# Kernel optimization log

Measured on AMD Instinct MI355X. Metric: run time of the kernel, lower is better.

The kernel has to match this reference:

```python
import jax, jax.numpy as jnp
import numpy as np

B, S, D, H, DH, F = 2, 2048, 1024, 16, 64, 4096
K = 2048  # number of selected tokens (capacity_gamma=0.5 of B*S)
EPS = 1e-6
ROPE_THETA = 10000.0


def setup_inputs() -> dict:
    key = jax.random.key(0)
    ks = jax.random.split(key, 12)
    w = lambda k, shp: jax.random.normal(k, shp, dtype=jnp.float32) * 0.02
    # K unique flat indices into the B*S token grid (every other token -> unique, sorted)
    sel_flat = jnp.arange(K, dtype=jnp.int64) * 2
    return {
        "hidden_states": jax.random.normal(ks[0], (B, S, D), dtype=jnp.float32),
        "gating_signal": jax.random.uniform(ks[1], (B, S), dtype=jnp.float32),
        "sel_flat": sel_flat,
        "position_ids": jnp.tile(jnp.arange(S, dtype=jnp.int64), (B, 1)),
        "ln1_w": jnp.ones((D,), jnp.float32),
        "ln2_w": jnp.ones((D,), jnp.float32),
        "wq": w(ks[2], (D, H * DH)), "bq": jnp.zeros((H * DH,), jnp.float32),
        "wk": w(ks[3], (D, H * DH)), "bk": jnp.zeros((H * DH,), jnp.float32),
        "wv": w(ks[4], (D, H * DH)), "bv": jnp.zeros((H * DH,), jnp.float32),
        "wo": w(ks[5], (H * DH, D)),
        "w_gate": w(ks[6], (D, F)),
        "w_up": w(ks[7], (D, F)),
        "w_down": w(ks[8], (F, D)),
    }


def _rmsnorm(x, w):
    var = jnp.mean(jnp.square(x), axis=-1, keepdims=True)
    return x * jax.lax.rsqrt(var + EPS) * w


def _rope(x, pos):
    # x: [K, H, DH], pos: [K]
    half = DH // 2
    inv_freq = 1.0 / (ROPE_THETA ** (jnp.arange(half, dtype=jnp.float32) / half))
    ang = pos.astype(jnp.float32)[:, None] * inv_freq  # [K, half]
    cos = jnp.cos(ang)[:, None, :]
    sin = jnp.sin(ang)[:, None, :]
    x1, x2 = x[..., :half], x[..., half:]
    return jnp.concatenate([x1 * cos - x2 * sin, x2 * cos + x1 * sin], axis=-1)


def reference(hidden_states, gating_signal, sel_flat, position_ids,
              ln1_w, ln2_w, wq, bq, wk, bk, wv, bv, wo, w_gate, w_up, w_down):
    b_idx = sel_flat // S
    t_idx = sel_flat % S

    # --- gather selected tokens ---
    x = hidden_states[b_idx, t_idx]          # [K, D]
    g = gating_signal[b_idx, t_idx]          # [K]
    pos = position_ids[b_idx, t_idx]         # [K]

    # --- Qwen2 block on the selected tokens (single sequence of length K) ---
    h = _rmsnorm(x, ln1_w)
    q = _rope((h @ wq + bq).reshape(K, H, DH), pos)
    k = _rope((h @ wk + bk).reshape(K, H, DH), pos)
    v = (h @ wv + bv).reshape(K, H, DH)

    scores = jnp.einsum("qhd,khd->hqk", q, k) / np.sqrt(DH)  # [H, K, K]
    causal = jnp.tril(jnp.ones((K, K), dtype=bool))
    scores = jnp.where(causal, scores, jnp.finfo(scores.dtype).min)
    probs = jax.nn.softmax(scores, axis=-1)
    attn = jnp.einsum("hqk,khd->qhd", probs, v).reshape(K, H * DH) @ wo

    x1 = x + attn
    h2 = _rmsnorm(x1, ln2_w)
    mlp = (jax.nn.silu(h2 @ w_gate) * (h2 @ w_up)) @ w_down
    y = x1 + mlp                              # processed tokens [K, D]

    # --- gated residual scatter-back ---
    updated = x + (y - x) * g[:, None]
    return hidden_states.at[b_idx, t_idx].set(updated)
```

## Files before the change

### kernel.cpp

```cpp
#include <hip/hip_runtime.h>
#include <hip/hip_bf16.h>
#include <stdint.h>

#define K_TOK 2048
#define D_DIM 1024
#define H_N   16
#define DH_N  64
#define F_DIM 4096
#define S_SEQ 2048

typedef __attribute__((ext_vector_type(4))) float f32x4;
typedef __attribute__((ext_vector_type(8))) short bf16x8;

__device__ __forceinline__ float bf2f(ushort u) {
  union { unsigned u; float f; } c; c.u = ((unsigned)u) << 16; return c.f;
}
__device__ __forceinline__ ushort f2bf(float f) {
  union { float f; unsigned u; } c; c.f = f;
  unsigned x = c.u + 0x7fffu + ((c.u >> 16) & 1u);
  return (ushort)(x >> 16);
}

#define GLOAD_LDS16(GP, LP)                                                   \
  __builtin_amdgcn_global_load_lds(                                           \
      (const __attribute__((address_space(1))) unsigned int*)(GP),            \
      (__attribute__((address_space(3))) unsigned int*)(LP), 16, 0, 0)

__global__ void copy_out_k(const float4* __restrict__ src, float4* __restrict__ dst, int n4) {
  int idx = blockIdx.x * blockDim.x + threadIdx.x;
  int stride = gridDim.x * blockDim.x;
  for (; idx < n4; idx += stride) dst[idx] = src[idx];
}

__global__ void prep_bias(const float* __restrict__ bq, const float* __restrict__ bk,
                          const float* __restrict__ bv, float* __restrict__ dst) {
  int i = blockIdx.x * 256 + threadIdx.x;
  if (i < 3072) dst[i] = (i < 1024) ? bq[i] : (i < 2048 ? bk[i - 1024] : bv[i - 2048]);
}

__global__ __launch_bounds__(256) void transpose_conv(const float* __restrict__ src,
                                                      ushort* __restrict__ dst,
                                                      int R, int C, int mul, int add, int ldd) {
  __shared__ float tile[32][33];
  int nbx = C >> 5;
  int bx = blockIdx.x % nbx, by = blockIdx.x / nbx;
  int c0 = bx << 5, r0 = by << 5;
  int tx = threadIdx.x & 31, ty = threadIdx.x >> 5;
#pragma unroll
  for (int i = 0; i < 32; i += 8)
    tile[ty + i][tx] = src[(size_t)(r0 + ty + i) * C + c0 + tx];
  __syncthreads();
#pragma unroll
  for (int i = 0; i < 32; i += 8) {
    int c = ty + i;
    dst[(size_t)((c0 + c) * mul + add) * ldd + r0 + tx] = f2bf(tile[tx][c]);
  }
}

__global__ __launch_bounds__(256) void gather_ln1(
    const float* __restrict__ hs, const float* __restrict__ gating,
    const int* __restrict__ sel32, const int* __restrict__ pos32,
    const float* __restrict__ w,
    float* __restrict__ xbuf, ushort* __restrict__ hbuf,
    float* __restrict__ gbuf, int* __restrict__ rowb, int* __restrict__ rowt,
    int* __restrict__ rowpos) {
  int i = blockIdx.x, tid = threadIdx.x;
  __shared__ float red[4];
  bool is64 = (sel32[1] == 0 && sel32[3] == 0 && sel32[5] == 0);
  int sel = is64 ? sel32[2 * i] : sel32[i];
  int b = sel >> 11;
  int t = sel & 2047;
  const float4* src = (const float4*)(hs + ((size_t)b * S_SEQ + t) * D_DIM);
  float4 v = src[tid];
  float ss = v.x * v.x + v.y * v.y + v.z * v.z + v.w * v.w;
  for (int off = 32; off; off >>= 1) ss += __shfl_xor(ss, off);
  if ((tid & 63) == 0) red[tid >> 6] = ss;
  __syncthreads();
  float tot = red[0] + red[1] + red[2] + red[3];
  float rms = rsqrtf(tot * (1.f / 1024.f) + 1e-6f);
  ((float4*)(xbuf + (size_t)i * D_DIM))[tid] = v;
  float4 lw = ((const float4*)w)[tid];
  ushort4 hv;
  hv.x = f2bf(v.x * rms * lw.x); hv.y = f2bf(v.y * rms * lw.y);
  hv.z = f2bf(v.z * rms * lw.z); hv.w = f2bf(v.w * rms * lw.w);
  *(ushort4*)&hbuf[(size_t)i * D_DIM + tid * 4] = hv;
  if (tid == 0) {
    rowb[i] = b; rowt[i] = t;
    bool is64p = (pos32[1] == 0 && pos32[3] == 0 && pos32[5] == 0);
    int pidx = b * S_SEQ + t;
    rowpos[i] = is64p ? pos32[2 * pidx] : pos32[pidx];
    gbuf[i] = gating[pidx];
  }
}

__global__ __launch_bounds__(256) void rmsnorm_ep1(const float* __restrict__ xbuf,
                                                   const float* __restrict__ pb,
                                                   const float* __restrict__ w,
                                                   float* __restrict__ x1out,
                                                   ushort* __restrict__ h2out) {
  int i = blockIdx.x, tid = threadIdx.x;
  __shared__ float red[4];
  size_t e = (size_t)i * D_DIM;
  float4 v = ((const float4*)(xbuf + e))[tid];
  float4 p0 = ((const float4*)(pb + e))[tid];
  float4 p1 = ((const float4*)(pb + 2097152 + e))[tid];
  v.x += p0.x + p1.x; v.y += p0.y + p1.y; v.z += p0.z + p1.z; v.w += p0.w + p1.w;
  ((float4*)(x1out + e))[tid] = v;
  float ss = v.x * v.x + v.y * v.y + v.z * v.z + v.w * v.w;
  for (int off = 32; off; off >>= 1) ss += __shfl_xor(ss, off);
  if ((tid & 63) == 0) red[tid >> 6] = ss;
  __syncthreads();
  float tot = red[0] + red[1] + red[2] + red[3];
  float rms = rsqrtf(tot * (1.f / 1024.f) + 1e-6f);
  float4 lw = ((const float4*)w)[tid];
  ushort4 hv;
  hv.x = f2bf(v.x * rms * lw.x); hv.y = f2bf(v.y * rms * lw.y);
  hv.z = f2bf(v.z * rms * lw.z); hv.w = f2bf(v.w * rms * lw.w);
  *(ushort4*)&h2out[e + tid * 4] = hv;
}

__global__ __launch_bounds__(256) void ep3_k(const float* __restrict__ pb,
                                             const float* __restrict__ x1b,
                                             const float* __restrict__ xbuf,
                                             const float* __restrict__ gbuf,
                                             const int* __restrict__ rowb,
                                             const int* __restrict__ rowt,
                                             float* __restrict__ out) {
  int idx = blockIdx.x * 256 + threadIdx.x;
  int row = idx >> 8, c4 = idx & 255;
  size_t e = (size_t)row * D_DIM + c4 * 4;
  float4 s0 = *(const float4*)(pb + e);
  float4 s1 = *(const float4*)(pb + 2097152 + e);
  float4 s2 = *(const float4*)(pb + 2 * 2097152 + e);
  float4 s3 = *(const float4*)(pb + 3 * 2097152 + e);
  float4 x = *(const float4*)(xbuf + e);
  float4 x1 = *(const float4*)(x1b + e);
  float g = gbuf[row];
  float4 r;
  r.x = x.x + (x1.x + s0.x + s1.x + s2.x + s3.x - x.x) * g;
  r.y = x.y + (x1.y + s0.y + s1.y + s2.y + s3.y - x.y) * g;
  r.z = x.z + (x1.z + s0.z + s1.z + s2.z + s3.z - x.z) * g;
  r.w = x.w + (x1.w + s0.w + s1.w + s2.w + s3.w - x.w) * g;
  *(float4*)(out + ((size_t)rowb[row] * S_SEQ + rowt[row]) * D_DIM + c4 * 4) = r;
}

template <int MODE>
__global__ __launch_bounds__(256) void gemm_bt(
    const ushort* __restrict__ A, const ushort* __restrict__ BT,
    int M, int N, int ldk, int kdeff, int per,
    const float* __restrict__ bias,
    ushort* __restrict__ outb, float* __restrict__ outf) {
  __shared__ ushort lA[128 * 64];
  __shared__ ushort lB[128 * 64];
  int tid = threadIdx.x;
  int lane = tid & 63, wid = tid >> 6;
  int kidx = blockIdx.x / per;
  int bid = blockIdx.x % per;
  int nbn = N >> 7;
  int tm = bid / nbn, tn = bid % nbn;
  int wr = wid >> 1, wc = wid & 1;
  f32x4 acc[4][4];
#pragma unroll
  for (int m = 0; m < 4; ++m)
#pragma unroll
    for (int n = 0; n < 4; ++n) acc[m][n] = (f32x4){0.f, 0.f, 0.f, 0.f};

  const ushort* Ab = A + (size_t)(tm * 128) * ldk + (size_t)kidx * kdeff;
  const ushort* Bb = BT + (size_t)(tn * 128) * ldk + (size_t)kidx * kdeff;
  int lr = lane & 15, lg = lane >> 4;
  int prow = lane >> 3;
  int pch = lane & 7;

  for (int k0 = 0; k0 < kdeff; k0 += 64) {
    __syncthreads();
#pragma unroll
    for (int p = 0; p < 4; ++p) {
      int row = p * 32 + wid * 8 + prow;
      int g = pch ^ (row & 7);
      GLOAD_LDS16(Ab + (size_t)row * ldk + k0 + g * 8, &lA[(p * 32 + wid * 8) * 64]);
      GLOAD_LDS16(Bb + (size_t)row * ldk + k0 + g * 8, &lB[(p * 32 + wid * 8) * 64]);
    }
    __syncthreads();
#pragma unroll
    for (int ks = 0; ks < 2; ++ks) {
      bf16x8 af[4], bfv[4];
#pragma unroll
      for (int m = 0; m < 4; ++m) {
        int row = wr * 64 + m * 16 + lr;
        af[m] = *(const bf16x8*)((const char*)lA + row * 128 +
                                 ((ks * 64 + lg * 16) ^ ((row & 7) << 4)));
      }
#pragma unroll
      for (int n = 0; n < 4; ++n) {
        int row = wc * 64 + n * 16 + lr;
        bfv[n] = *(const bf16x8*)((const char*)lB + row * 128 +
                                  ((ks * 64 + lg * 16) ^ ((row & 7) << 4)));
      }
#pragma unroll
      for (int m = 0; m < 4; ++m)
#pragma unroll
        for (int n = 0; n < 4; ++n)
          acc[m][n] = __builtin_amdgcn_mfma_f32_16x16x32_bf16(af[m], bfv[n], acc[m][n], 0, 0, 0);
    }
  }

#pragma unroll
  for (int m = 0; m < 4; ++m) {
#pragma unroll
    for (int n = 0; n < 4; ++n) {
#pragma unroll
      for (int r = 0; r < 4; ++r) {
        int gr = tm * 128 + wr * 64 + m * 16 + lg * 4 + r;
        int gc = tn * 128 + wc * 64 + n * 16 + lr;
        float val = acc[m][n][r];
        if (MODE == 0) {
          outb[(size_t)gr * N + gc] = f2bf(val + bias[gc]);
        } else if (MODE == 2) {
          float other = __shfl_xor(val, 1);
          if (!(lane & 1)) {
            float g = val, u = other;
            float a = g / (1.f + __expf(-g)) * u;
            outb[(size_t)gr * (size_t)(N >> 1) + (gc >> 1)] = f2bf(a);
          }
        } else {
          outf[((size_t)kidx * M + gr) * N + gc] = val;
        }
      }
    }
  }
}

__global__ __launch_bounds__(256) void rope_kernel(const ushort* __restrict__ qkv,
                                                   const int* __restrict__ rowpos,
                                                   ushort* __restrict__ qr,
                                                   ushort* __restrict__ kr) {
  int idx = blockIdx.x * 256 + threadIdx.x;
  int i = idx >> 9;
  int rem = idx & 511;
  int h = rem >> 5, d = rem & 31;
  float pos = (float)rowpos[i];
  float inv = __expf(-(float)d * (9.210340371976184f / 32.0f));
  float ang = pos * inv;
  float sn, cs;
  __sincosf(ang, &sn, &cs);
  size_t base = (size_t)i * 3072;
  float q1 = bf2f(qkv[base + h * 64 + d]);
  float q2 = bf2f(qkv[base + h * 64 + 32 + d]);
  float k1 = bf2f(qkv[base + 1024 + h * 64 + d]);
  float k2 = bf2f(qkv[base + 1024 + h * 64 + 32 + d]);
  size_t ob = ((size_t)h * K_TOK + i) * DH_N;
  qr[ob + d] = f2bf((q1 * cs - q2 * sn) * 0.125f);
  qr[ob + 32 + d] = f2bf((q2 * cs + q1 * sn) * 0.125f);
  kr[ob + d] = f2bf(k1 * cs - k2 * sn);
  kr[ob + 32 + d] = f2bf(k2 * cs + k1 * sn);
}

__global__ __launch_bounds__(256) void vtrans_k(const ushort* __restrict__ qkv,
                                                ushort* __restrict__ vt) {
  __shared__ ushort tile[32][33];
  int bx = blockIdx.x & 63, by = blockIdx.x >> 6;
  int i0 = bx << 5, c0 = by << 5;
  int tx = threadIdx.x & 31, ty = threadIdx.x >> 5;
#pragma unroll
  for (int j = 0; j < 32; j += 8)
    tile[ty + j][tx] = qkv[(size_t)(i0 + ty + j) * 3072 + 2048 + c0 + tx];
  __syncthreads();
#pragma unroll
  for (int j = 0; j < 32; j += 8)
    vt[(size_t)(c0 + ty + j) * K_TOK + i0 + tx] = tile[tx][ty + j];
}

__global__ __launch_bounds__(256) void attn_mfma(const ushort* __restrict__ qr,
                                                 const ushort* __restrict__ kr,
                                                 const ushort* __restrict__ vt,
                                                 ushort* __restrict__ ows,
                                                 float* __restrict__ mlws) {
  __shared__ ushort ktile[2][64 * 64];
  __shared__ ushort vtile[2][64 * 64];
  __shared__ ushort pbuf[4][16 * 64];
  int tid = threadIdx.x, lane = tid & 63, wid = tid >> 6;
  int bid = blockIdx.x;
  int h = bid / 144;
  int rem = 143 - (bid % 144);
  int g = 0;
  while (rem >= 2 * (g + 1) * (g + 2)) ++g;
  int rem2 = rem - 2 * g * (g + 1);
  int qt = (g << 2) + rem2 / (g + 1);
  int ci = rem2 % (g + 1);
  int slot = h * 144 + rem;
  int q0 = qt << 6;
  int t0 = ci << 2;
  int t1 = min(t0 + 3, qt);

  const ushort* Kh = kr + (size_t)h * K_TOK * DH_N;
  const ushort* Vh = vt + (size_t)h * DH_N * K_TOK;
  int lr = lane & 15, lg = lane >> 4;
  int qbase = q0 + wid * 16;

  bf16x8 qf[2];
  const ushort* Qp = qr + ((size_t)h * K_TOK + qbase + lr) * DH_N + lg * 8;
  qf[0] = *(const bf16x8*)(Qp);
  qf[1] = *(const bf16x8*)(Qp + 32);

  f32x4 oa[4];
  float mreg[4], lreg[4];
#pragma unroll
  for (int ct = 0; ct < 4; ++ct) oa[ct] = (f32x4){0.f, 0.f, 0.f, 0.f};
#pragma unroll
  for (int r = 0; r < 4; ++r) { mreg[r] = -1e30f; lreg[r] = 0.f; }

  char* pws = (char*)&pbuf[wid][0];
  int srow8 = lane >> 3, schunk = lane & 7;

  auto stage = [&](int bi, int kb) {
#pragma unroll
    for (int j = 0; j < 2; ++j) {
      int rbase = wid * 16 + j * 8;
      int row = rbase + srow8;
      int gch = schunk ^ (row & 7);
      GLOAD_LDS16(Kh + (size_t)(kb + row) * DH_N + gch * 8, &ktile[bi][rbase * 64]);
      GLOAD_LDS16(Vh + (size_t)row * K_TOK + kb + gch * 8, &vtile[bi][rbase * 64]);
    }
  };

  stage(0, t0 << 6);
  int cur = 0;
  for (int t = t0; t <= t1; ++t) {
    int kb = t << 6;
    __syncthreads();
    if (t < t1) stage(cur ^ 1, (t + 1) << 6);

    const char* kt = (const char*)&ktile[cur][0];
    const char* vtl = (const char*)&vtile[cur][0];

    f32x4 sa[4];
#pragma unroll
    for (int ct = 0; ct < 4; ++ct) sa[ct] = (f32x4){0.f, 0.f, 0.f, 0.f};
#pragma unroll
    for (int s = 0; s < 2; ++s) {
#pragma unroll
      for (int ct = 0; ct < 4; ++ct) {
        int row = ct * 16 + lr;
        bf16x8 kf = *(const bf16x8*)(kt + row * 128 + ((s * 64 + lg * 16) ^ ((row & 7) << 4)));
        sa[ct] = __builtin_amdgcn_mfma_f32_16x16x32_bf16(qf[s], kf, sa[ct], 0, 0, 0);
      }
    }

#pragma unroll
    for (int r = 0; r < 4; ++r) {
      int q = qbase + lg * 4 + r;
      int prow = lg * 4 + r;
      float sv[4];
      float mx = mreg[r];
#pragma unroll
      for (int ct = 0; ct < 4; ++ct) {
        int key = kb + ct * 16 + lr;
        float x = sa[ct][r];
        sv[ct] = (key <= q) ? x : -1e30f;
        mx = fmaxf(mx, sv[ct]);
      }
      mx = fmaxf(mx, __shfl_xor(mx, 1));
      mx = fmaxf(mx, __shfl_xor(mx, 2));
      mx = fmaxf(mx, __shfl_xor(mx, 4));
      mx = fmaxf(mx, __shfl_xor(mx, 8));
      float resc = __expf(mreg[r] - mx);
      float ps = 0.f;
#pragma unroll
      for (int ct = 0; ct < 4; ++ct) {
        float p = __expf(sv[ct] - mx);
        ps += p;
        *(ushort*)(pws + prow * 128 + ((ct * 32 + lr * 2) ^ ((prow & 7) << 4))) = f2bf(p);
      }
      ps += __shfl_xor(ps, 1);
      ps += __shfl_xor(ps, 2);
      ps += __shfl_xor(ps, 4);
      ps += __shfl_xor(ps, 8);
      lreg[r] = lreg[r] * resc + ps;
      mreg[r] = mx;
#pragma unroll
      for (int ct = 0; ct < 4; ++ct) oa[ct][r] *= resc;
    }

    bf16x8 pf[2];
#pragma unroll
    for (int s = 0; s < 2; ++s)
      pf[s] = *(const bf16x8*)(pws + lr * 128 + ((s * 64 + lg * 16) ^ ((lr & 7) << 4)));
#pragma unroll
    for (int s = 0; s < 2; ++s) {
#pragma unroll
      for (int ct = 0; ct < 4; ++ct) {
        int row = ct * 16 + lr;
        bf16x8 vf = *(const bf16x8*)(vtl + row * 128 + ((s * 64 + lg * 16) ^ ((row & 7) << 4)));
        oa[ct] = __builtin_amdgcn_mfma_f32_16x16x32_bf16(pf[s], vf, oa[ct], 0, 0, 0);
      }
    }
    cur ^= 1;
  }

#pragma unroll
  for (int ct = 0; ct < 4; ++ct) {
#pragma unroll
    for (int r = 0; r < 4; ++r) {
      int prow = wid * 16 + lg * 4 + r;
      ows[(size_t)slot * 4096 + prow * 64 + ct * 16 + lr] = f2bf(oa[ct][r]);
    }
  }
  if (lr == 0) {
#pragma unroll
    for (int r = 0; r < 4; ++r) {
      int prow = wid * 16 + lg * 4 + r;
      mlws[(size_t)slot * 128 + prow] = mreg[r];
      mlws[(size_t)slot * 128 + 64 + prow] = lreg[r];
    }
  }
}

__global__ __launch_bounds__(256) void attn_combine(const ushort* __restrict__ ows,
                                                    const float* __restrict__ mlws,
                                                    ushort* __restrict__ aout) {
  int bid = blockIdx.x;
  int h = bid & 15, qt = bid >> 4;
  int g = qt >> 2;
  int nc = g + 1;
  int base = h * 144 + 2 * g * (g + 1) + (qt & 3) * nc;
  int tid = threadIdx.x;
  int row = tid >> 2, c0 = (tid & 3) * 16;
  float M = -1e30f;
  for (int i = 0; i < nc; ++i)
    M = fmaxf(M, mlws[(size_t)(base + i) * 128 + row]);
  float L = 0.f;
  float acc[16];
#pragma unroll
  for (int j = 0; j < 16; ++j) acc[j] = 0.f;
  for (int i = 0; i < nc; ++i) {
    size_t sl = (size_t)(base + i);
    float w = __expf(mlws[sl * 128 + row] - M);
    L += mlws[sl * 128 + 64 + row] * w;
    const bf16x8* op = (const bf16x8*)(ows + sl * 4096 + row * 64 + c0);
    bf16x8 v0 = op[0], v1 = op[1];
#pragma unroll
    for (int j = 0; j < 8; ++j) acc[j] += bf2f(((ushort)v0[j])) * w;
#pragma unroll
    for (int j = 0; j < 8; ++j) acc[8 + j] += bf2f(((ushort)v1[j])) * w;
  }
  float inv = 1.f / L;
  int q = qt * 64 + row;
  ushort* dst = aout + (size_t)q * D_DIM + h * DH_N + c0;
#pragma unroll
  for (int j = 0; j < 16; ++j) dst[j] = f2bf(acc[j] * inv);
}

extern "C" void kernel_launch(void* const* d_in, const int* in_sizes, int n_in,
                              void* d_out, int out_size, void* d_ws, size_t ws_size,
                              hipStream_t stream) {
  const float* hs = (const float*)d_in[0];
  const float* gating = (const float*)d_in[1];
  const int* sel32 = (const int*)d_in[2];
  const int* pos32 = (const int*)d_in[3];
  const float* ln1w = (const float*)d_in[4];
  const float* ln2w = (const float*)d_in[5];
  const float* wq = (const float*)d_in[6];
  const float* bq = (const float*)d_in[7];
  const float* wk = (const float*)d_in[8];
  const float* bk = (const float*)d_in[9];
  const float* wv = (const float*)d_in[10];
  const float* bv = (const float*)d_in[11];
  const float* wo = (const float*)d_in[12];
  const float* wg = (const float*)d_in[13];
  const float* wu = (const float*)d_in[14];
  const float* wd = (const float*)d_in[15];
  float* out = (float*)d_out;

  char* wsb = (char*)d_ws;
  size_t off = 0;
  auto alloc = [&](size_t bytes) -> void* {
    void* p = wsb + off;
    off += (bytes + 255) & ~(size_t)255;
    return p;
  };
  ushort* qkvT = (ushort*)alloc(3072ull * 1024 * 2);
  ushort* woT = (ushort*)alloc(1024ull * 1024 * 2);
  ushort* guT = (ushort*)alloc(8192ull * 1024 * 2);
  ushort* wdT = (ushort*)alloc(1024ull * 4096 * 2);
  float* biasqkv = (float*)alloc(3072 * 4);
  float* xbuf = (float*)alloc(2048ull * 1024 * 4);
  ushort* hbuf = (ushort*)alloc(2048ull * 1024 * 2);
  ushort* qkv = (ushort*)alloc(2048ull * 3072 * 2);
  ushort* qrb = (ushort*)alloc(16ull * 2048 * 64 * 2);
  ushort* krb = (ushort*)alloc(16ull * 2048 * 64 * 2);
  ushort* vtb = (ushort*)alloc(16ull * 64 * 2048 * 2);
  ushort* aoutb = (ushort*)alloc(2048ull * 1024 * 2);
  float* pbuf = (float*)hbuf;
  float* x1b = (float*)alloc(2048ull * 1024 * 4);
  ushort* h2b = (ushort*)alloc(2048ull * 1024 * 2);
  ushort* actb = (ushort*)alloc(2048ull * 4096 * 2);
  ushort* aows = (ushort*)x1b;
  float* amlws = (float*)((char*)x1b + 2304ull * 4096 * 2);
  float* gbuf = (float*)alloc(2048 * 4);
  int* rowb = (int*)alloc(2048 * 4);
  int* rowt = (int*)alloc(2048 * 4);
  int* rowpos = (int*)alloc(2048 * 4);
  if (off > ws_size) return;

  copy_out_k<<<2048, 256, 0, stream>>>((const float4*)hs, (float4*)out, (2 * S_SEQ * D_DIM) / 4);
  prep_bias<<<12, 256, 0, stream>>>(bq, bk, bv, biasqkv);
  transpose_conv<<<1024, 256, 0, stream>>>(wq, qkvT, 1024, 1024, 1, 0, 1024);
  transpose_conv<<<1024, 256, 0, stream>>>(wk, qkvT + 1024 * 1024, 1024, 1024, 1, 0, 1024);
  transpose_conv<<<1024, 256, 0, stream>>>(wv, qkvT + 2048 * 1024, 1024, 1024, 1, 0, 1024);
  transpose_conv<<<1024, 256, 0, stream>>>(wo, woT, 1024, 1024, 1, 0, 1024);
  transpose_conv<<<4096, 256, 0, stream>>>(wg, guT, 1024, 4096, 2, 0, 1024);
  transpose_conv<<<4096, 256, 0, stream>>>(wu, guT, 1024, 4096, 2, 1, 1024);
  transpose_conv<<<4096, 256, 0, stream>>>(wd, wdT, 4096, 1024, 1, 0, 4096);
  gather_ln1<<<2048, 256, 0, stream>>>(hs, gating, sel32, pos32, ln1w, xbuf, hbuf, gbuf, rowb,
                                       rowt, rowpos);
  gemm_bt<0><<<16 * 24, 256, 0, stream>>>(hbuf, qkvT, 2048, 3072, 1024, 1024, 16 * 24, biasqkv,
                                          qkv, nullptr);
  rope_kernel<<<4096, 256, 0, stream>>>(qkv, rowpos, qrb, krb);
  vtrans_k<<<2048, 256, 0, stream>>>(qkv, vtb);
  attn_mfma<<<16 * 144, 256, 0, stream>>>(qrb, krb, vtb, aows, amlws);
  attn_combine<<<512, 256, 0, stream>>>(aows, amlws, aoutb);
  gemm_bt<4><<<2 * 16 * 8, 256, 0, stream>>>(aoutb, woT, 2048, 1024, 1024, 512, 16 * 8, nullptr,
                                             nullptr, pbuf);
  rmsnorm_ep1<<<2048, 256, 0, stream>>>(xbuf, pbuf, ln2w, x1b, h2b);
  gemm_bt<2><<<16 * 64, 256, 0, stream>>>(h2b, guT, 2048, 8192, 1024, 1024, 16 * 64, nullptr,
                                          actb, nullptr);
  gemm_bt<4><<<4 * 16 * 8, 256, 0, stream>>>(actb, wdT, 2048, 1024, 4096, 1024, 16 * 8, nullptr,
                                             nullptr, pbuf);
  ep3_k<<<2048, 256, 0, stream>>>(pbuf, x1b, xbuf, gbuf, rowb, rowt, out);
}
```

Before: 229.9 us.

## Use 256x256-tile double-buffered GEMM for gate/up and vectorize weight transposes

Replaces the generic 128x128 gate/up GEMM with a dedicated 512-thread kernel that computes 256x256 tiles, using double-buffered direct-to-LDS loads, XOR-swizzled LDS reads, s_setprio around the MFMA block and a block-index swizzle for L2 locality. The fused SiLU*up epilogue is kept. The weight transpose kernel now works on 64x64 tiles with float4 loads and ushort4 stores, which cuts the block count and the number of memory transactions. The larger tile gives more operand reuse per LDS load, but needs many more accumulator registers and leaves only 256 blocks, which could limit occupancy.

Result: no change. 229.9 us (+0.0%).

```diff
diff --git a/kernel.cpp b/kernel.cpp
--- a/kernel.cpp
+++ b/kernel.cpp
@@ -38,22 +38,29 @@
   if (i < 3072) dst[i] = (i < 1024) ? bq[i] : (i < 2048 ? bk[i - 1024] : bv[i - 2048]);
 }
 
-__global__ __launch_bounds__(256) void transpose_conv(const float* __restrict__ src,
-                                                      ushort* __restrict__ dst,
-                                                      int R, int C, int mul, int add, int ldd) {
-  __shared__ float tile[32][33];
-  int nbx = C >> 5;
+__global__ __launch_bounds__(256) void transpose_conv64(const float* __restrict__ src,
+                                                        ushort* __restrict__ dst,
+                                                        int R, int C, int mul, int add, int ldd) {
+  __shared__ float tile[64][65];
+  int nbx = C >> 6;
   int bx = blockIdx.x % nbx, by = blockIdx.x / nbx;
-  int c0 = bx << 5, r0 = by << 5;
-  int tx = threadIdx.x & 31, ty = threadIdx.x >> 5;
-#pragma unroll
-  for (int i = 0; i < 32; i += 8)
-    tile[ty + i][tx] = src[(size_t)(r0 + ty + i) * C + c0 + tx];
+  int c0 = bx << 6, r0 = by << 6;
+  int tx = threadIdx.x & 15, ty = threadIdx.x >> 4;
+#pragma unroll
+  for (int i = 0; i < 4; ++i) {
+    float4 v = *(const float4*)&src[(size_t)(r0 + ty + i * 16) * C + c0 + tx * 4];
+    *(float4*)&tile[ty + i * 16][tx * 4] = v;
+  }
   __syncthreads();
 #pragma unroll
-  for (int i = 0; i < 32; i += 8) {
-    int c = ty + i;
-    dst[(size_t)((c0 + c) * mul + add) * ldd + r0 + tx] = f2bf(tile[tx][c]);
+  for (int i = 0; i < 4; ++i) {
+    int c = ty + i * 16;
+    ushort4 o;
+    o.x = f2bf(tile[tx * 4 + 0][c]);
+    o.y = f2bf(tile[tx * 4 + 1][c]);
+    o.z = f2bf(tile[tx * 4 + 2][c]);
+    o.w = f2bf(tile[tx * 4 + 3][c]);
+    *(ushort4*)&dst[(size_t)((c0 + c) * mul + add) * ldd + r0 + tx * 4] = o;
   }
 }
 
@@ -215,19 +222,106 @@
         float val = acc[m][n][r];
         if (MODE == 0) {
           outb[(size_t)gr * N + gc] = f2bf(val + bias[gc]);
-        } else if (MODE == 2) {
-          float other = __shfl_xor(val, 1);
-          if (!(lane & 1)) {
-            float g = val, u = other;
-            float a = g / (1.f + __expf(-g)) * u;
-            outb[(size_t)gr * (size_t)(N >> 1) + (gc >> 1)] = f2bf(a);
-          }
         } else {
           outf[((size_t)kidx * M + gr) * N + gc] = val;
         }
       }
     }
   }
+}
+
+__global__ __launch_bounds__(512, 2) void gemm256_gu(const ushort* __restrict__ A,
+                                                     const ushort* __restrict__ BT,
+                                                     ushort* __restrict__ outb) {
+  __shared__ ushort lA[2][256 * 32];
+  __shared__ ushort lB[2][256 * 32];
+  int tid = threadIdx.x, lane = tid & 63, wid = tid >> 6;
+  int bid = blockIdx.x;
+  int sb = (bid & 7) * 32 + (bid >> 3);
+  int tm = sb >> 5, tn = sb & 31;
+  int wm = wid >> 2, wn = wid & 3;
+  int lr = lane & 15, lg = lane >> 4;
+  const ushort* Ab = A + (size_t)(tm * 256) * 1024;
+  const ushort* Bb = BT + (size_t)(tn * 256) * 1024;
+  int srow = lane >> 2, sch = lane & 3;
+
+  f32x4 acc[8][4];
+#pragma unroll
+  for (int m = 0; m < 8; ++m)
+#pragma unroll
+    for (int n = 0; n < 4; ++n) acc[m][n] = (f32x4){0.f, 0.f, 0.f, 0.f};
+
+#define STAGE_GU(bi, t)                                                        \
+  {                                                                            \
+    int k0 = (t) * 32;                                                         \
+    _Pragma("unroll") for (int j = 0; j < 2; ++j) {                            \
+      int R = j * 128 + wid * 16;                                              \
+      int row = R + srow;                                                      \
+      int g = sch ^ (row & 3);                                                 \
+      GLOAD_LDS16(Ab + (size_t)row * 1024 + k0 + g * 8, &lA[bi][R * 32]);      \
+      GLOAD_LDS16(Bb + (size_t)row * 1024 + k0 + g * 8, &lB[bi][R * 32]);      \
+    }                                                                          \
+  }
+
+  STAGE_GU(0, 0);
+  STAGE_GU(1, 1);
+  asm volatile("s_waitcnt vmcnt(4)" ::: "memory");
+  __syncthreads();
+
+  for (int t = 0; t < 32; ++t) {
+    int c = t & 1;
+    bf16x8 af[8], bfr[4];
+#pragma unroll
+    for (int m = 0; m < 8; ++m) {
+      int row = wm * 128 + m * 16 + lr;
+      af[m] = *(const bf16x8*)((const char*)&lA[c][0] + row * 64 +
+                               ((lg * 16) ^ ((row & 3) << 4)));
+    }
+#pragma unroll
+    for (int n = 0; n < 4; ++n) {
+      int row = wn * 64 + n * 16 + lr;
+      bfr[n] = *(const bf16x8*)((const char*)&lB[c][0] + row * 64 +
+                                ((lg * 16) ^ ((row & 3) << 4)));
+    }
+    asm volatile("s_waitcnt lgkmcnt(0)" ::: "memory");
+    __syncthreads();
+    if (t + 2 < 32) STAGE_GU(c, t + 2);
+    __builtin_amdgcn_sched_barrier(0);
+    __builtin_amdgcn_s_setprio(1);
+#pragma unroll
+    for (int m = 0; m < 8; ++m)
+#pragma unroll
+      for (int n = 0; n < 4; ++n)
+        acc[m][n] = __builtin_amdgcn_mfma_f32_16x16x32_bf16(af[m], bfr[n], acc[m][n], 0, 0, 0);
+    __builtin_amdgcn_s_setprio(0);
+    if (t + 1 < 32) {
+      if (t + 2 < 32)
+        asm volatile("s_waitcnt vmcnt(4)" ::: "memory");
+      else
+        asm volatile("s_waitcnt vmcnt(0)" ::: "memory");
+      __syncthreads();
+    }
+  }
+
+#pragma unroll
+  for (int m = 0; m < 8; ++m) {
+#pragma unroll
+    for (int n = 0; n < 4; ++n) {
+#pragma unroll
+      for (int r = 0; r < 4; ++r) {
+        int gr = tm * 256 + wm * 128 + m * 16 + lg * 4 + r;
+        int gc = tn * 256 + wn * 64 + n * 16 + lr;
+        float val = acc[m][n][r];
+        float other = __shfl_xor(val, 1);
+        if (!(lane & 1)) {
+          float g = val, u = other;
+          float a = g / (1.f + __expf(-g)) * u;
+          outb[(size_t)gr * (F_DIM) + (gc >> 1)] = f2bf(a);
+        }
+      }
+    }
+  }
+#undef STAGE_GU
 }
 
 __global__ __launch_bounds__(256) void rope_kernel(const ushort* __restrict__ qkv,
@@ -504,13 +598,13 @@
 
   copy_out_k<<<2048, 256, 0, stream>>>((const float4*)hs, (float4*)out, (2 * S_SEQ * D_DIM) / 4);
   prep_bias<<<12, 256, 0, stream>>>(bq, bk, bv, biasqkv);
-  transpose_conv<<<1024, 256, 0, stream>>>(wq, qkvT, 1024, 1024, 1, 0, 1024);
-  transpose_conv<<<1024, 256, 0, stream>>>(wk, qkvT + 1024 * 1024, 1024, 1024, 1, 0, 1024);
-  transpose_conv<<<1024, 256, 0, stream>>>(wv, qkvT + 2048 * 1024, 1024, 1024, 1, 0, 1024);
-  transpose_conv<<<1024, 256, 0, stream>>>(wo, woT, 1024, 1024, 1, 0, 1024);
-  transpose_conv<<<4096, 256, 0, stream>>>(wg, guT, 1024, 4096, 2, 0, 1024);
-  transpose_conv<<<4096, 256, 0, stream>>>(wu, guT, 1024, 4096, 2, 1, 1024);
-  transpose_conv<<<4096, 256, 0, stream>>>(wd, wdT, 4096, 1024, 1, 0, 4096);
+  transpose_conv64<<<256, 256, 0, stream>>>(wq, qkvT, 1024, 1024, 1, 0, 1024);
+  transpose_conv64<<<256, 256, 0, stream>>>(wk, qkvT + 1024 * 1024, 1024, 1024, 1, 0, 1024);
+  transpose_conv64<<<256, 256, 0, stream>>>(wv, qkvT + 2048 * 1024, 1024, 1024, 1, 0, 1024);
+  transpose_conv64<<<256, 256, 0, stream>>>(wo, woT, 1024, 1024, 1, 0, 1024);
+  transpose_conv64<<<1024, 256, 0, stream>>>(wg, guT, 1024, 4096, 2, 0, 1024);
+  transpose_conv64<<<1024, 256, 0, stream>>>(wu, guT, 1024, 4096, 2, 1, 1024);
+  transpose_conv64<<<1024, 256, 0, stream>>>(wd, wdT, 4096, 1024, 1, 0, 4096);
   gather_ln1<<<2048, 256, 0, stream>>>(hs, gating, sel32, pos32, ln1w, xbuf, hbuf, gbuf, rowb,
                                        rowt, rowpos);
   gemm_bt<0><<<16 * 24, 256, 0, stream>>>(hbuf, qkvT, 2048, 3072, 1024, 1024, 16 * 24, biasqkv,
@@ -522,8 +616,7 @@
   gemm_bt<4><<<2 * 16 * 8, 256, 0, stream>>>(aoutb, woT, 2048, 1024, 1024, 512, 16 * 8, nullptr,
                                              nullptr, pbuf);
   rmsnorm_ep1<<<2048, 256, 0, stream>>>(xbuf, pbuf, ln2w, x1b, h2b);
-  gemm_bt<2><<<16 * 64, 256, 0, stream>>>(h2b, guT, 2048, 8192, 1024, 1024, 16 * 64, nullptr,
-                                          actb, nullptr);
+  gemm256_gu<<<256, 512, 0, stream>>>(h2b, guT, actb);
   gemm_bt<4><<<4 * 16 * 8, 256, 0, stream>>>(actb, wdT, 2048, 1024, 4096, 1024, 16 * 8, nullptr,
                                              nullptr, pbuf);
   ep3_k<<<2048, 256, 0, stream>>>(pbuf, x1b, xbuf, gbuf, rowb, rowt, out);
```
